# Kernel tuning notes

Measured on AMD Instinct MI355X. Metric: run time of the kernel, lower is better.

The kernel has to match this reference:

```python
import jax, jax.numpy as jnp
import numpy as np

OC, IC, K, STRIDE, PAD, DIL, GROUPS = 256, 256, 3, 1, 1, 1, 1


def _conv_one(x, w):
    # x: [C, H, W], w: [OC, IC//groups, K, K]
    out = jax.lax.conv_general_dilated(
        x[None], w,
        window_strides=(STRIDE, STRIDE),
        padding=[(PAD, PAD), (PAD, PAD)],
        rhs_dilation=(DIL, DIL),
        dimension_numbers=("NCHW", "OIHW", "NCHW"),
        feature_group_count=GROUPS,
    )
    return out[0]  # [OC, H', W']


def setup_inputs() -> dict:
    key = jax.random.key(0)
    k1, k2, k3, k4 = jax.random.split(key, 4)
    B, num = 32, 64
    inputs = jax.random.normal(k1, (B, IC, 56, 56), dtype=jnp.float32)
    inputs_se = jax.random.normal(k2, (B, num), dtype=jnp.float32)
    fan = IC * K * K
    weight = jax.random.normal(k3, (OC * IC * K * K // GROUPS, num), dtype=jnp.float32) / np.sqrt(num * fan)
    bias = jax.random.normal(k4, (OC,), dtype=jnp.float32) * 0.01
    return {"inputs": inputs, "inputs_se": inputs_se, "weight": weight, "bias": bias}


def reference(inputs, inputs_se, weight, bias):
    B = inputs.shape[0]
    # per-sample weight synthesis: [B, OC*IC*K*K//groups]
    w = jnp.einsum("bn,on->bo", inputs_se, weight)
    w = w.reshape(B, OC, IC // GROUPS, K, K)
    out = jax.vmap(_conv_one)(inputs, w)  # [B, OC, H', W']
    return out + bias.reshape(1, -1, 1, 1)
```

## Files before the change

### kernel.cpp

```cpp
#include <hip/hip_runtime.h>

typedef __bf16 bf16x8 __attribute__((ext_vector_type(8)));
typedef float  f32x4  __attribute__((ext_vector_type(4)));

#define B_   32
#define OC   256
#define IC   256
#define HW   3136
#define HP   60
#define WP   58
#define KTOT 2304
#define XPAD_BYTES ((size_t)B_ * HP * WP * IC * 2)

__device__ __forceinline__ void async16(const void* g, void* l) {
    __builtin_amdgcn_global_load_lds(
        (__attribute__((address_space(1))) void*)g,
        (__attribute__((address_space(3))) void*)l, 16, 0, 0);
}

__global__ __launch_bounds__(256) void zero_border(__bf16* __restrict__ Xpad) {
    int t   = blockIdx.x * 256 + threadIdx.x;
    int b   = t / 11008;
    int r2  = t - b * 11008;
    int pos = r2 >> 5, iq = r2 & 31;
    int r, c;
    if (pos < 232) { int rr = pos / 58; c = pos - rr * 58; r = (rr == 0) ? 0 : (56 + rr); }
    else           { int p2 = pos - 232; r = 1 + (p2 >> 1); c = (p2 & 1) * 57; }
    uint4 z = make_uint4(0u, 0u, 0u, 0u);
    *(uint4*)(Xpad + ((size_t)b * (HP * WP) + r * WP + c) * IC + iq * 8) = z;
}

__global__ __launch_bounds__(256) void transpose_pad(
    const float* __restrict__ X, __bf16* __restrict__ Xpad) {
    int sc = blockIdx.x, icc = blockIdx.y, b = blockIdx.z;
    __shared__ float lt[64][65];
    int tid = threadIdx.x;
    {
        int ci = tid >> 2, sq = tid & 3;
        const float* src = X + (size_t)(b * IC + icc * 64 + ci) * HW + sc * 64 + sq * 16;
        float4 v0 = ((const float4*)src)[0];
        float4 v1 = ((const float4*)src)[1];
        float4 v2 = ((const float4*)src)[2];
        float4 v3 = ((const float4*)src)[3];
        float* dst = &lt[ci][sq * 16];
        ((float4*)dst)[0] = v0; ((float4*)dst)[1] = v1;
        ((float4*)dst)[2] = v2; ((float4*)dst)[3] = v3;
    }
    __syncthreads();
    {
        int p = tid >> 2, iq = tid & 3;
        int s = sc * 64 + p;
        int h = s / 56, w = s - h * 56;
        __bf16* dst = Xpad + ((size_t)b * (HP * WP) + (h + 1) * WP + (w + 1)) * IC + icc * 64 + iq * 16;
        bf16x8 v0, v1;
        #pragma unroll
        for (int j = 0; j < 8; ++j) v0[j] = (__bf16)lt[iq * 16 + j][p];
        #pragma unroll
        for (int j = 0; j < 8; ++j) v1[j] = (__bf16)lt[iq * 16 + 8 + j][p];
        *(bf16x8*)dst = v0;
        *(bf16x8*)(dst + 8) = v1;
    }
}

__global__ __launch_bounds__(256) void synth(
    const float* __restrict__ se, const float* __restrict__ weight,
    __bf16* __restrict__ Asyn) {
    int oc = blockIdx.x / 9, tap = blockIdx.x - oc * 9;
    int tid = threadIdx.x;
    const float* wrow = weight + ((size_t)(oc * 256 + tid) * 9 + tap) * 64;
    float4 w[16];
    #pragma unroll
    for (int i = 0; i < 16; ++i) w[i] = ((const float4*)wrow)[i];
    size_t outb = (size_t)oc * KTOT + tap * 256 + tid;
    #pragma unroll
    for (int b = 0; b < 32; ++b) {
        const float4* sb = (const float4*)(se + b * 64);
        float acc = 0.f;
        #pragma unroll
        for (int i = 0; i < 16; ++i) {
            float4 s4 = sb[i];
            acc += w[i].x * s4.x + w[i].y * s4.y + w[i].z * s4.z + w[i].w * s4.w;
        }
        Asyn[(size_t)b * OC * KTOT + outb] = (__bf16)acc;
    }
}

__global__ __launch_bounds__(256) void conv_mfma(
    const __bf16* __restrict__ Asyn, const __bf16* __restrict__ Xpad,
    const float* __restrict__ bias, float* __restrict__ Out) {
    const int i = blockIdx.x;
    const int xcd = i & 7, slot = i >> 3;
    const int bg = slot / 50, r2 = slot - bg * 50;
    const int b = xcd + 8 * bg;
    const int mtile = r2 & 1, ntile = r2 >> 1;

    __shared__ __bf16 Al[128 * 64];
    __shared__ __bf16 Bl[128 * 64];
    const int tid = threadIdx.x;
    const int wid = tid >> 6, lane = tid & 63;

    const int rsub = lane >> 3;
    const int q = (lane & 7) ^ rsub;
    const __bf16* ap[4]; const __bf16* bp[4];
    char* alds[4]; char* blds[4];
    const __bf16* xb = Xpad + (size_t)b * (HP * WP) * IC;
    #pragma unroll
    for (int c = 0; c < 4; ++c) {
        const int r = wid * 32 + c * 8 + rsub;
        ap[c] = Asyn + (size_t)(b * OC + mtile * 128 + r) * KTOT + q * 8;
        const int nn = ntile * 128 + r;
        const int h = nn / 56, w = nn - h * 56;
        bp[c] = xb + (h * WP + w) * IC + q * 8;
        alds[c] = (char*)Al + (wid * 32 + c * 8) * 128;
        blds[c] = (char*)Bl + (wid * 32 + c * 8) * 128;
    }

    const int wm = wid & 1, wn = wid >> 1;
    const int fr = lane & 15, fq = lane >> 4;
    int aoff[4], boff[4];
    #pragma unroll
    for (int i2 = 0; i2 < 4; ++i2) {
        const int ra = wm * 64 + i2 * 16 + fr;
        aoff[i2] = ra * 128 + ((fq ^ (ra & 7)) * 16);
        const int rb = wn * 64 + i2 * 16 + fr;
        boff[i2] = rb * 128 + ((fq ^ (rb & 7)) * 16);
    }
    f32x4 acc[4][4] = {};

    for (int tap = 0; tap < 9; ++tap) {
        const int kh = tap / 3, kw = tap - kh * 3;
        const int boB = (kh * WP + kw) * IC;
        const int aoA = tap * 256;
        #pragma unroll
        for (int sub = 0; sub < 4; ++sub) {
            const int ka = aoA + sub * 64;
            const int kb = boB + sub * 64;
            #pragma unroll
            for (int c = 0; c < 4; ++c) async16(ap[c] + ka, alds[c]);
            #pragma unroll
            for (int c = 0; c < 4; ++c) async16(bp[c] + kb, blds[c]);
            __syncthreads();
            #pragma unroll
            for (int t = 0; t < 2; ++t) {
                bf16x8 af[4], bv[4];
                #pragma unroll
                for (int i2 = 0; i2 < 4; ++i2) {
                    af[i2] = *(const bf16x8*)((char*)Al + (aoff[i2] ^ (t * 64)));
                    bv[i2] = *(const bf16x8*)((char*)Bl + (boff[i2] ^ (t * 64)));
                }
                #pragma unroll
                for (int mi = 0; mi < 4; ++mi)
                    #pragma unroll
                    for (int ni = 0; ni < 4; ++ni)
                        acc[mi][ni] = __builtin_amdgcn_mfma_f32_16x16x32_bf16(
                            af[mi], bv[ni], acc[mi][ni], 0, 0, 0);
            }
            __syncthreads();
        }
    }

    #pragma unroll
    for (int mi = 0; mi < 4; ++mi) {
        #pragma unroll
        for (int r = 0; r < 4; ++r) {
            const int row = mtile * 128 + wm * 64 + mi * 16 + fq * 4 + r;
            const float bvv = bias[row];
            float* orow = Out + (size_t)(b * OC + row) * HW;
            #pragma unroll
            for (int ni = 0; ni < 4; ++ni) {
                const int col = ntile * 128 + wn * 64 + ni * 16 + fr;
                if (col < HW) orow[col] = acc[mi][ni][r] + bvv;
            }
        }
    }
}

extern "C" void kernel_launch(void* const* d_in, const int* in_sizes, int n_in,
                              void* d_out, int out_size, void* d_ws, size_t ws_size,
                              hipStream_t stream) {
    const float* X    = (const float*)d_in[0];
    const float* se   = (const float*)d_in[1];
    const float* Wt   = (const float*)d_in[2];
    const float* bias = (const float*)d_in[3];
    __bf16* Xpad = (__bf16*)d_ws;
    __bf16* Asyn = (__bf16*)((char*)d_ws + XPAD_BYTES);
    float*  Out  = (float*)d_out;

    zero_border<<<1376, 256, 0, stream>>>(Xpad);
    transpose_pad<<<dim3(49, 4, 32), 256, 0, stream>>>(X, Xpad);
    synth<<<2304, 256, 0, stream>>>(se, Wt, Asyn);
    conv_mfma<<<1600, 256, 0, stream>>>(Asyn, Xpad, bias, Out);
}
```

Measured before the change: 512.9 us.

## Use per-wave LDS double buffering and direct global B loads in conv

The conv kernel drops the block-wide shared A/B tiles and the two __syncthreads per k-step. Each wave now loads its B fragments straight from global memory into registers and stages its own A slice through a private double-buffered LDS region. The next A slice is prefetched asynchronously, guarded only by a vmcnt wait, and launch bounds now request 3 blocks per CU. This removes block barriers and LDS traffic for B. In exchange, B fragments are duplicated across the waves that share them, global reads go up, and the asynchronous LDS ordering becomes fragile.

```diff
diff --git a/kernel.cpp b/kernel.cpp
--- a/kernel.cpp
+++ b/kernel.cpp
@@ -85,7 +85,7 @@
     }
 }
 
-__global__ __launch_bounds__(256) void conv_mfma(
+__global__ __launch_bounds__(256, 3) void conv_mfma(
     const __bf16* __restrict__ Asyn, const __bf16* __restrict__ Xpad,
     const float* __restrict__ bias, float* __restrict__ Out) {
     const int i = blockIdx.x;
@@ -94,69 +94,60 @@
     const int b = xcd + 8 * bg;
     const int mtile = r2 & 1, ntile = r2 >> 1;
 
-    __shared__ __bf16 Al[128 * 64];
-    __shared__ __bf16 Bl[128 * 64];
+    __shared__ __bf16 Al[4][2][2048];
     const int tid = threadIdx.x;
     const int wid = tid >> 6, lane = tid & 63;
+    const int wm = wid & 1, wn = wid >> 1;
+    const int fr = lane & 15, fq = lane >> 4;
 
-    const int rsub = lane >> 3;
-    const int q = (lane & 7) ^ rsub;
-    const __bf16* ap[4]; const __bf16* bp[4];
-    char* alds[4]; char* blds[4];
-    const __bf16* xb = Xpad + (size_t)b * (HP * WP) * IC;
+    const __bf16* ap[4];
     #pragma unroll
     for (int c = 0; c < 4; ++c) {
-        const int r = wid * 32 + c * 8 + rsub;
-        ap[c] = Asyn + (size_t)(b * OC + mtile * 128 + r) * KTOT + q * 8;
-        const int nn = ntile * 128 + r;
+        const int row = mtile * 128 + wm * 64 + c * 16 + (lane >> 2);
+        ap[c] = Asyn + (size_t)(b * OC + row) * KTOT + (lane & 3) * 8;
+    }
+    const __bf16* xb = Xpad + (size_t)b * (HP * WP) * IC;
+    const __bf16* xbn[4];
+    #pragma unroll
+    for (int i2 = 0; i2 < 4; ++i2) {
+        const int nn = ntile * 128 + wn * 64 + i2 * 16 + fr;
         const int h = nn / 56, w = nn - h * 56;
-        bp[c] = xb + (h * WP + w) * IC + q * 8;
-        alds[c] = (char*)Al + (wid * 32 + c * 8) * 128;
-        blds[c] = (char*)Bl + (wid * 32 + c * 8) * 128;
+        xbn[i2] = xb + (h * WP + w) * IC + fq * 8;
     }
 
-    const int wm = wid & 1, wn = wid >> 1;
-    const int fr = lane & 15, fq = lane >> 4;
-    int aoff[4], boff[4];
+    f32x4 acc[4][4] = {};
+    char* mybuf = (char*)&Al[wid][0][0];
+
     #pragma unroll
-    for (int i2 = 0; i2 < 4; ++i2) {
-        const int ra = wm * 64 + i2 * 16 + fr;
-        aoff[i2] = ra * 128 + ((fq ^ (ra & 7)) * 16);
-        const int rb = wn * 64 + i2 * 16 + fr;
-        boff[i2] = rb * 128 + ((fq ^ (rb & 7)) * 16);
-    }
-    f32x4 acc[4][4] = {};
+    for (int c = 0; c < 4; ++c) async16(ap[c], mybuf + c * 1024);
 
-    for (int tap = 0; tap < 9; ++tap) {
-        const int kh = tap / 3, kw = tap - kh * 3;
-        const int boB = (kh * WP + kw) * IC;
-        const int aoA = tap * 256;
+    #pragma unroll 2
+    for (int k = 0; k < 72; ++k) {
+        const int tap = k >> 3, icc = k & 7;
+        const int kh = (tap * 11) >> 5;
+        const int kw = tap - kh * 3;
+        const int offB = (kh * WP + kw) * IC + icc * 32;
+        bf16x8 bv[4];
         #pragma unroll
-        for (int sub = 0; sub < 4; ++sub) {
-            const int ka = aoA + sub * 64;
-            const int kb = boB + sub * 64;
+        for (int i2 = 0; i2 < 4; ++i2)
+            bv[i2] = *(const bf16x8*)(xbn[i2] + offB);
+        const int kn = (k < 71) ? k + 1 : 71;
+        const int offA = ((kn >> 3) << 8) + ((kn & 7) << 5);
+        char* nbuf = mybuf + ((k + 1) & 1) * 4096;
+        #pragma unroll
+        for (int c = 0; c < 4; ++c) async16(ap[c] + offA, nbuf + c * 1024);
+        __builtin_amdgcn_s_waitcnt(0x0f74);
+        bf16x8 af[4];
+        const char* rbuf = mybuf + (k & 1) * 4096;
+        #pragma unroll
+        for (int i2 = 0; i2 < 4; ++i2)
+            af[i2] = *(const bf16x8*)(rbuf + (i2 * 16 + fr) * 64 + fq * 16);
+        #pragma unroll
+        for (int mi = 0; mi < 4; ++mi)
             #pragma unroll
-            for (int c = 0; c < 4; ++c) async16(ap[c] + ka, alds[c]);
-            #pragma unroll
-            for (int c = 0; c < 4; ++c) async16(bp[c] + kb, blds[c]);
-            __syncthreads();
-            #pragma unroll
-            for (int t = 0; t < 2; ++t) {
-                bf16x8 af[4], bv[4];
-                #pragma unroll
-                for (int i2 = 0; i2 < 4; ++i2) {
-                    af[i2] = *(const bf16x8*)((char*)Al + (aoff[i2] ^ (t * 64)));
-                    bv[i2] = *(const bf16x8*)((char*)Bl + (boff[i2] ^ (t * 64)));
-                }
-                #pragma unroll
-                for (int mi = 0; mi < 4; ++mi)
-                    #pragma unroll
-                    for (int ni = 0; ni < 4; ++ni)
-                        acc[mi][ni] = __builtin_amdgcn_mfma_f32_16x16x32_bf16(
-                            af[mi], bv[ni], acc[mi][ni], 0, 0, 0);
-            }
-            __syncthreads();
-        }
+            for (int ni = 0; ni < 4; ++ni)
+                acc[mi][ni] = __builtin_amdgcn_mfma_f32_16x16x32_bf16(
+                    af[mi], bv[ni], acc[mi][ni], 0, 0, 0);
     }
 
     #pragma unroll
```

New measurement: 651.1 us. 1.27x slower.
